# Performance work log

Hardware: AMD Instinct MI355X
Metric: run time of the kernel (lower is better)

Reference implementation:

```python
import jax, jax.numpy as jnp
import numpy as np

B, L, D_INNER, D_STATE, DT_RANK, MODES = 4, 2048, 256, 16, 16, 32
LN_EPS = 1e-5


def setup_inputs() -> dict:
    key = jax.random.key(0)
    ks = jax.random.split(key, 10)
    x = jax.random.normal(ks[0], (B, L, D_INNER), dtype=jnp.float32)
    ln_g = jnp.ones((D_INNER,), jnp.float32)
    ln_b = jnp.zeros((D_INNER,), jnp.float32)
    W_xproj = jax.random.normal(ks[1], (DT_RANK + 2 * D_STATE, D_INNER), jnp.float32) * (D_INNER ** -0.5)
    dt_init_std = DT_RANK ** -0.5  # dt_scale = 1.0
    W_dt = jax.random.uniform(ks[2], (D_INNER, DT_RANK), jnp.float32, -dt_init_std, dt_init_std)
    dt = jnp.exp(jax.random.uniform(ks[3], (D_INNER,), jnp.float32) * (np.log(0.1) - np.log(0.001)) + np.log(0.001))
    dt = jnp.clip(dt, 1e-4, None)
    b_dt = dt + jnp.log(-jnp.expm1(-dt))  # inverse softplus
    A_log = jnp.zeros((D_INNER, D_STATE), jnp.float32)  # log(ones)
    D_param = jnp.ones((D_INNER,), jnp.float32)
    scale = 1.0 / (D_STATE * D_STATE)
    w_re = scale * jax.random.uniform(ks[4], (D_STATE, D_STATE, MODES), jnp.float32)
    w_im = scale * jax.random.uniform(ks[5], (D_STATE, D_STATE, MODES), jnp.float32)
    return {"x": x, "ln_g": ln_g, "ln_b": ln_b, "W_xproj": W_xproj, "W_dt": W_dt,
            "b_dt": b_dt, "A_log": A_log, "D_param": D_param, "w_re": w_re, "w_im": w_im}


def _fft_kernel(hs, w_re, w_im):
    # hs: (B, L, d_inner, d_state); rfft over d_inner with d_state channels
    h = jnp.transpose(hs, (0, 1, 3, 2))  # (B, L, k, N)
    hf = jnp.fft.rfft(h, axis=-1)        # (B, L, k, N//2+1) complex
    n_freq = D_INNER // 2 + 1
    l = min(MODES, n_freq)
    w = (w_re + 1j * w_im).astype(hf.dtype)
    of = jnp.einsum('blix,iox->blox', hf[..., :l], w[..., :l])
    of = jnp.pad(of, ((0, 0), (0, 0), (0, 0), (0, n_freq - l)))
    h2 = jnp.fft.irfft(of, n=D_INNER, axis=-1)  # real, (B, L, k, N)
    return jnp.transpose(h2, (0, 1, 3, 2))      # (B, L, d_inner, d_state)


def reference(x, ln_g, ln_b, W_xproj, W_dt, b_dt, A_log, D_param, w_re, w_im):
    # LayerNorm
    mu = jnp.mean(x, axis=-1, keepdims=True)
    var = jnp.var(x, axis=-1, keepdims=True)
    xn = (x - mu) * jax.lax.rsqrt(var + LN_EPS) * ln_g + ln_b

    A = -jnp.exp(A_log)  # (d_inner, d_state)
    dbc = xn @ W_xproj.T  # (B, L, dt_rank + 2*d_state)
    delta_r = dbc[..., :DT_RANK]
    Bc = dbc[..., DT_RANK:DT_RANK + D_STATE]        # (B, L, d_state)
    Cc = dbc[..., DT_RANK + D_STATE:]               # (B, L, d_state)
    delta = jax.nn.softplus(delta_r @ W_dt.T + b_dt)  # (B, L, d_inner)

    deltaA = jnp.exp(delta[..., None] * A)                       # (B, L, d_inner, d_state)
    BX = delta[..., None] * Bc[:, :, None, :] * xn[..., None]    # (B, L, d_inner, d_state)

    # selective scan: h_t = deltaA_t * h_{t-1} + BX_t (parallel associative scan over L)
    def comb(c1, c2):
        a1, b1 = c1
        a2, b2 = c2
        return a1 * a2, a2 * b1 + b2
    _, hs = jax.lax.associative_scan(comb, (deltaA, BX), axis=1)

    hs = _fft_kernel(hs, w_re, w_im)
    y = jnp.einsum('bldn,bln->bld', hs, Cc)  # hs @ C
    y = y + D_param * xn
    return y + x
```

## Files before the change

kernel.cpp:

```cpp
#include <hip/hip_runtime.h>
#include <hip/hip_bf16.h>

#define B_   4
#define L_   2048
#define D_   256
#define NC   128
#define CL   16
#define ANG  0.02454369260617025967f

typedef __bf16 bf16x8 __attribute__((ext_vector_type(8)));
typedef float  f32x4  __attribute__((ext_vector_type(4)));

__global__ __launch_bounds__(256) void k_prep(
        const float* __restrict__ W_xproj, const float* __restrict__ w_re, const float* __restrict__ w_im,
        __hip_bfloat16* __restrict__ E_t, __hip_bfloat16* __restrict__ Wfrag,
        __hip_bfloat16* __restrict__ wfrag, __hip_bfloat16* __restrict__ E_inv)
{
    int idx = blockIdx.x * 256 + threadIdx.x;
    if (idx < 16384) {
        int x = idx >> 8, d = idx & 255;
        float v = (x < 32) ? __cosf(ANG * (float)((x * d) & 255))
                           : -__sinf(ANG * (float)(((x - 32) * d) & 255));
        E_t[idx] = __float2bfloat16(v);
    } else if (idx < 32768) {
        int f = idx - 16384;
        int ks = f >> 11, t = (f >> 3) & 255, j = f & 7;
        int jcol = (t >> 6) * 16 + (t & 15);
        int dd = ks * 32 + ((t >> 4) & 3) * 8 + j;
        float v = (jcol < 48) ? W_xproj[jcol * 256 + dd] : 0.f;
        Wfrag[f] = __float2bfloat16(v);
    } else if (idx < 65536) {
        int f = idx - 32768;
        int nt = f >> 9, l = (f >> 3) & 63, j = f & 7;
        int n = nt * 16 + (l & 15);
        int o = ((l >> 4) & 3) * 8 + j;
        float v = 0.f;
        if (o < 16) {
            int i = n >> 6, comp = (n >> 5) & 1, x = n & 31;
            v = comp ? w_im[(i * 16 + o) * 32 + x] : w_re[(i * 16 + o) * 32 + x];
        }
        wfrag[f] = __float2bfloat16(v);
    } else if (idx < 81920) {
        int f = idx - 65536;
        int nt = f >> 10, ks = (f >> 9) & 1, l = (f >> 3) & 63, j = f & 7;
        int row = ks * 32 + ((l >> 4) & 3) * 8 + j;
        int col = nt * 16 + (l & 15);
        float v = (row < 32) ? __cosf(ANG * (float)((row * col) & 255))
                             : -__sinf(ANG * (float)(((row - 32) * col) & 255));
        E_inv[f] = __float2bfloat16(v);
    }
}

__global__ __launch_bounds__(256) void k_lnscan(
        const float* __restrict__ x, const float* __restrict__ ln_g, const float* __restrict__ ln_b,
        const float* __restrict__ W_dt, const float* __restrict__ b_dt,
        const float* __restrict__ D_param, const float* __restrict__ A_log,
        const __hip_bfloat16* __restrict__ Wfrag,
        unsigned int* __restrict__ dxn, float* __restrict__ base_o,
        float* __restrict__ Bc_o, float* __restrict__ Cc_o,
        float* __restrict__ P, float* __restrict__ S)
{
    __shared__ __align__(16) float xn_s[16 * 260];
    __shared__ __align__(16) __bf16 xnb[16 * 256];
    __shared__ float dbc_s[16 * 52];
    int tid = threadIdx.x, wave = tid >> 6, lane = tid & 63;
    int blk = blockIdx.x;
    int grow0 = blk * CL;
    char* xnb_c = (char*)xnb;

#pragma unroll
    for (int rr = 0; rr < 4; rr++) {
        int r = wave * 4 + rr;
        const float* xr = x + (size_t)(grow0 + r) * D_;
        float v[4];
#pragma unroll
        for (int q = 0; q < 4; q++) v[q] = xr[lane + q * 64];
        float sum = v[0] + v[1] + v[2] + v[3];
        float sq  = v[0]*v[0] + v[1]*v[1] + v[2]*v[2] + v[3]*v[3];
#pragma unroll
        for (int off = 32; off; off >>= 1) { sum += __shfl_xor(sum, off); sq += __shfl_xor(sq, off); }
        float mu = sum * (1.f / D_);
        float rstd = rsqrtf(sq * (1.f / D_) - mu * mu + 1e-5f);
#pragma unroll
        for (int q = 0; q < 4; q++) {
            int d = lane + q * 64;
            float xv = (v[q] - mu) * rstd * ln_g[d] + ln_b[d];
            xn_s[r * 260 + d] = xv;
            *(__bf16*)(xnb_c + r * 512 + ((d * 2) ^ ((r & 7) << 4))) = (__bf16)xv;
            base_o[(size_t)(grow0 + r) * D_ + d] = v[q] + D_param[d] * xv;
        }
    }
    __syncthreads();

    {
        int mrow = lane & 15;
        f32x4 acc = {0.f, 0.f, 0.f, 0.f};
#pragma unroll
        for (int ks = 0; ks < 8; ks++) {
            bf16x8 af = *(const bf16x8*)(xnb_c + mrow * 512 +
                          ((ks * 64 + ((lane >> 4) * 16)) ^ ((mrow & 7) << 4)));
            bf16x8 bf = *(const bf16x8*)(Wfrag + (ks * 256 + tid) * 8);
            acc = __builtin_amdgcn_mfma_f32_16x16x32_bf16(af, bf, acc, 0, 0, 0);
        }
        int j = wave * 16 + (lane & 15);
#pragma unroll
        for (int q = 0; q < 4; q++) {
            int r = (lane >> 4) * 4 + q;
            if (j < 48) dbc_s[r * 52 + j] = acc[q];
            if (j >= 32 && j < 48)      Cc_o[(size_t)(grow0 + r) * 16 + j - 32] = acc[q];
            else if (j >= 16 && j < 32) Bc_o[(size_t)(grow0 + r) * 16 + j - 16] = acc[q];
        }
    }
    __syncthreads();

    int d = tid;
    float wdt[16];
#pragma unroll
    for (int q = 0; q < 4; q++) {
        f32x4 w4 = *(const f32x4*)&W_dt[d * 16 + q * 4];
#pragma unroll
        for (int k = 0; k < 4; k++) wdt[q * 4 + k] = w4[k];
    }
    float bd = b_dt[d];
    float dlt_r[16];
#pragma unroll
    for (int r = 0; r < 16; r++) {
        float din = bd;
#pragma unroll
        for (int k = 0; k < 16; k++) din = fmaf(dbc_s[r * 52 + k], wdt[k], din);
        din = (din > 15.f) ? din : log1pf(__expf(din));
        dlt_r[r] = din;
        union { __bf16 h2[2]; unsigned int u; } pk;
        pk.h2[0] = (__bf16)din;
        pk.h2[1] = (__bf16)xn_s[r * 260 + d];
        dxn[(size_t)(grow0 + r) * D_ + d] = pk.u;
    }

    float ar[16];
#pragma unroll
    for (int q = 0; q < 4; q++) {
        f32x4 a4 = *(const f32x4*)&A_log[d * 16 + q * 4];
#pragma unroll
        for (int k = 0; k < 4; k++) ar[q * 4 + k] = -__expf(a4[k]);
    }
    bool uni = true;
#pragma unroll
    for (int n = 1; n < 16; n++) uni = uni && (ar[n] == ar[0]);
    float s[16], dsum = 0.f;
#pragma unroll
    for (int n = 0; n < 16; n++) s[n] = 0.f;
    if (uni) {
        float ar0 = ar[0];
#pragma unroll
        for (int t = 0; t < CL; t++) {
            float dl = dlt_r[t];
            float dx = dl * xn_s[t * 260 + d];
            dsum += dl;
            float e = __expf(dl * ar0);
#pragma unroll
            for (int n = 0; n < 16; n++)
                s[n] = fmaf(e, s[n], dx * dbc_s[t * 52 + 16 + n]);
        }
    } else {
#pragma unroll
        for (int t = 0; t < CL; t++) {
            float dl = dlt_r[t];
            float dx = dl * xn_s[t * 260 + d];
            dsum += dl;
#pragma unroll
            for (int n = 0; n < 16; n++) {
                float e = __expf(dl * ar[n]);
                s[n] = fmaf(e, s[n], dx * dbc_s[t * 52 + 16 + n]);
            }
        }
    }
    size_t o = (size_t)blk * 4096 + d * 16;
    if (uni) {
        float p0 = __expf(ar[0] * dsum);
#pragma unroll
        for (int q = 0; q < 4; q++) {
            f32x4 pv, sv;
#pragma unroll
            for (int k = 0; k < 4; k++) { pv[k] = p0; sv[k] = s[q*4+k]; }
            *reinterpret_cast<f32x4*>(&P[o + q * 4]) = pv;
            *reinterpret_cast<f32x4*>(&S[o + q * 4]) = sv;
        }
    } else {
#pragma unroll
        for (int q = 0; q < 4; q++) {
            f32x4 pv, sv;
#pragma unroll
            for (int k = 0; k < 4; k++) { pv[k] = __expf(ar[q*4+k] * dsum); sv[k] = s[q*4+k]; }
            *reinterpret_cast<f32x4*>(&P[o + q * 4]) = pv;
            *reinterpret_cast<f32x4*>(&S[o + q * 4]) = sv;
        }
    }
}

__global__ __launch_bounds__(256) void k_scan_par(
        const float* __restrict__ P, float* __restrict__ S_H0)
{
    __shared__ float gPS[512];
    int tid = threadIdx.x;
    int g2 = tid >> 5, cl2 = tid & 31;
    int ch = blockIdx.x * 32 + cl2;
    int b2 = ch >> 12, dn2 = ch & 4095;
    size_t cb = ((size_t)b2 * NC + g2 * 16) * 4096 + dn2;
    float pv[16], sv[16];
#pragma unroll
    for (int c = 0; c < 16; c++) {
        pv[c] = P[cb + (size_t)c * 4096];
        sv[c] = S_H0[cb + (size_t)c * 4096];
    }
    float pA = 1.f, sA = 0.f;
#pragma unroll
    for (int c = 0; c < 16; c++) { sA = fmaf(pv[c], sA, sv[c]); pA *= pv[c]; }
    gPS[(g2 * 32 + cl2) * 2 - (g2 * 32 + cl2)] = 0.f;
    gPS[(g2 * 32 + cl2)] = pA;
    __syncthreads();
    __shared__ float gS2[256];
    gS2[g2 * 32 + cl2] = sA;
    __syncthreads();
    float h = 0.f;
    for (int gg = 0; gg < g2; gg++)
        h = fmaf(gPS[gg * 32 + cl2], h, gS2[gg * 32 + cl2]);
#pragma unroll
    for (int c = 0; c < 16; c++) {
        S_H0[cb + (size_t)c * 4096] = h;
        h = fmaf(pv[c], h, sv[c]);
    }
}

__global__ __launch_bounds__(256, 2) void k_fused(
        const unsigned int* __restrict__ dxn,
        const float* __restrict__ Bc, const float* __restrict__ Cc,
        const float* __restrict__ A_log, const float* __restrict__ H0,
        const float* __restrict__ base, float* __restrict__ out,
        const __hip_bfloat16* __restrict__ E_t, const __hip_bfloat16* __restrict__ wfrag,
        const __hip_bfloat16* __restrict__ E_inv)
{
    __shared__ __align__(16) char smem[70784];
    __bf16* hfb  = (__bf16*)(smem + 32768);
    __bf16* gsb  = (__bf16*)(smem + 66560);
    __bf16* ccb  = (__bf16*)(smem + 68736);
    float*  bc_s = (float*)(smem + 69760);

    int tid = threadIdx.x, wave = tid >> 6, lane = tid & 63;
    int blk = blockIdx.x;
    int grow0 = blk * CL;
    int d = tid;

    bc_s[tid] = Bc[(size_t)grow0 * 16 + tid];
    {
        float ccv = Cc[(size_t)grow0 * 16 + tid];
        int r = tid >> 4, o = tid & 15;
        ccb[r * 32 + o] = (__bf16)ccv;
        ccb[r * 32 + 16 + o] = (__bf16)0.f;
    }
    float dlt[16], dxv[16];
#pragma unroll
    for (int t = 0; t < 16; t++) {
        unsigned int v = dxn[(size_t)(grow0 + t) * D_ + d];
        dlt[t] = __uint_as_float(v << 16);
        dxv[t] = __uint_as_float(v & 0xffff0000u);
    }
    float ar[16], h[16];
    {
        size_t ho = (size_t)blk * 4096 + d * 16;
#pragma unroll
        for (int q = 0; q < 4; q++) {
            f32x4 a4 = *(const f32x4*)&A_log[d * 16 + q * 4];
            f32x4 h4 = *(const f32x4*)&H0[ho + q * 4];
#pragma unroll
            for (int k = 0; k < 4; k++) { ar[q*4+k] = -__expf(a4[k]); h[q*4+k] = h4[k]; }
        }
    }
    bool uni = true;
#pragma unroll
    for (int n = 1; n < 16; n++) uni = uni && (ar[n] == ar[0]);
    float ar0 = ar[0];

    int xx = wave * 16 + (lane & 15);
    bf16x8 bfrag[8];
#pragma unroll
    for (int ks = 0; ks < 8; ks++)
        bfrag[ks] = *(const bf16x8*)(E_t + xx * 256 + ks * 32 + ((lane >> 4) * 8));
    int swz = (lane & 7) << 4;
    __syncthreads();

#pragma unroll
    for (int g = 0; g < 4; g++) {
        if (uni) {
#pragma unroll
            for (int tl = 0; tl < 4; tl++) {
                int t = g * 4 + tl;
                float dl = dlt[t];
                float dx = dl * dxv[t];
                float e = __expf(dl * ar0);
#pragma unroll
                for (int n = 0; n < 16; n++) {
                    h[n] = fmaf(e, h[n], dx * bc_s[t * 16 + n]);
                    int m = tl * 16 + n;
                    *(__bf16*)(smem + m * 512 + ((d * 2) ^ ((m & 7) << 4))) = (__bf16)h[n];
                }
            }
        } else {
#pragma unroll
            for (int tl = 0; tl < 4; tl++) {
                int t = g * 4 + tl;
                float dl = dlt[t];
                float dx = dl * dxv[t];
#pragma unroll
                for (int n = 0; n < 16; n++) {
                    float e = __expf(dl * ar[n]);
                    h[n] = fmaf(e, h[n], dx * bc_s[t * 16 + n]);
                    int m = tl * 16 + n;
                    *(__bf16*)(smem + m * 512 + ((d * 2) ^ ((m & 7) << 4))) = (__bf16)h[n];
                }
            }
        }
        __syncthreads();
        f32x4 acc[4];
#pragma unroll
        for (int mt = 0; mt < 4; mt++) { acc[mt][0]=0.f; acc[mt][1]=0.f; acc[mt][2]=0.f; acc[mt][3]=0.f; }
#pragma unroll
        for (int ks = 0; ks < 8; ks++) {
#pragma unroll
            for (int mt = 0; mt < 4; mt++) {
                int m = mt * 16 + (lane & 15);
                bf16x8 af = *(const bf16x8*)(smem + m * 512 + ((ks * 64 + ((lane >> 4) * 16)) ^ swz));
                acc[mt] = __builtin_amdgcn_mfma_f32_16x16x32_bf16(af, bfrag[ks], acc[mt], 0, 0, 0);
            }
        }
#pragma unroll
        for (int mt = 0; mt < 4; mt++) {
            int r = g * 4 + mt;
#pragma unroll
            for (int q = 0; q < 4; q++) {
                int i = (lane >> 4) * 4 + q;
                hfb[(r * 16 + i) * 66 + xx] = (__bf16)acc[mt][q];
            }
        }
        __syncthreads();
    }

    {
        bf16x8 ccf = *(const bf16x8*)((char*)ccb + (lane & 15) * 64 + ((lane >> 4) * 16));
#pragma unroll
        for (int ntl = 0; ntl < 16; ntl++) {
            int nt = wave * 16 + ntl;
            f32x4 a = {0.f, 0.f, 0.f, 0.f};
            bf16x8 wf = *(const bf16x8*)(wfrag + (nt * 64 + lane) * 8);
            a = __builtin_amdgcn_mfma_f32_16x16x32_bf16(ccf, wf, a, 0, 0, 0);
            int col = nt * 16 + (lane & 15);
#pragma unroll
            for (int q = 0; q < 4; q++) {
                int r = (lane >> 4) * 4 + q;
                *(__bf16*)(smem + r * 2048 + col * 2) = (__bf16)a[q];
            }
        }
    }
    __syncthreads();

    {
        int xs = tid & 31, rg = tid >> 5;
#pragma unroll
        for (int r2 = 0; r2 < 2; r2++) {
            int r = rg * 2 + r2;
            float gre = 0.f, gim = 0.f;
#pragma unroll
            for (int i = 0; i < 16; i++) {
                float hr = (float)hfb[(r * 16 + i) * 66 + xs];
                float hi = (float)hfb[(r * 16 + i) * 66 + 32 + xs];
                float wr = (float)*(__bf16*)(smem + r * 2048 + (i * 64 + xs) * 2);
                float wi = (float)*(__bf16*)(smem + r * 2048 + (i * 64 + 32 + xs) * 2);
                gre = fmaf(hr, wr, gre); gre = fmaf(-hi, wi, gre);
                gim = fmaf(hr, wi, gim); gim = fmaf(hi, wr, gim);
            }
            float sc = xs ? 2.f : 1.f;
            gsb[r * 68 + xs]      = (__bf16)(gre * sc);
            gsb[r * 68 + 32 + xs] = (__bf16)(gim * sc);
        }
    }
    __syncthreads();

    {
        bf16x8 ga0 = *(const bf16x8*)((char*)gsb + (lane & 15) * 136 + ((lane >> 4) * 16));
        bf16x8 ga1 = *(const bf16x8*)((char*)gsb + (lane & 15) * 136 + 64 + ((lane >> 4) * 16));
#pragma unroll
        for (int ntl = 0; ntl < 4; ntl++) {
            int nt = wave * 4 + ntl;
            f32x4 a = {0.f, 0.f, 0.f, 0.f};
            a = __builtin_amdgcn_mfma_f32_16x16x32_bf16(
                    ga0, *(const bf16x8*)(E_inv + ((nt * 2 + 0) * 64 + lane) * 8), a, 0, 0, 0);
            a = __builtin_amdgcn_mfma_f32_16x16x32_bf16(
                    ga1, *(const bf16x8*)(E_inv + ((nt * 2 + 1) * 64 + lane) * 8), a, 0, 0, 0);
            int dcol = nt * 16 + (lane & 15);
#pragma unroll
            for (int q = 0; q < 4; q++) {
                int r = (lane >> 4) * 4 + q;
                size_t go = (size_t)(grow0 + r) * D_ + dcol;
                out[go] = base[go] + a[q] * (1.f / 256.f);
            }
        }
    }
}

extern "C" void kernel_launch(void* const* d_in, const int* in_sizes, int n_in,
                              void* d_out, int out_size, void* d_ws, size_t ws_size,
                              hipStream_t stream)
{
    const float* x       = (const float*)d_in[0];
    const float* ln_g    = (const float*)d_in[1];
    const float* ln_b    = (const float*)d_in[2];
    const float* W_xproj = (const float*)d_in[3];
    const float* W_dt    = (const float*)d_in[4];
    const float* b_dt    = (const float*)d_in[5];
    const float* A_log   = (const float*)d_in[6];
    const float* D_param = (const float*)d_in[7];
    const float* w_re    = (const float*)d_in[8];
    const float* w_im    = (const float*)d_in[9];

    float* ws    = (float*)d_ws;
    float* base  = ws;
    float* S_H0  = base + 2097152;
    float* P     = S_H0 + 2097152;
    unsigned int* dxn = (unsigned int*)(P + 2097152);
    float* Bc    = (float*)(dxn + 2097152);
    float* Cc    = Bc + 131072;
    __hip_bfloat16* tab = (__hip_bfloat16*)(Cc + 131072);
    __hip_bfloat16* E_t   = tab;
    __hip_bfloat16* Wfrag = tab + 16384;
    __hip_bfloat16* wfrag = tab + 32768;
    __hip_bfloat16* E_inv = tab + 65536;
    float* out = (float*)d_out;

    hipLaunchKernelGGL(k_prep, dim3(320), dim3(256), 0, stream,
                       W_xproj, w_re, w_im, E_t, Wfrag, wfrag, E_inv);
    hipLaunchKernelGGL(k_lnscan, dim3(B_*NC), dim3(256), 0, stream,
                       x, ln_g, ln_b, W_dt, b_dt, D_param, A_log, Wfrag,
                       dxn, base, Bc, Cc, P, S_H0);
    hipLaunchKernelGGL(k_scan_par, dim3(B_*NC), dim3(256), 0, stream, P, S_H0);
    hipLaunchKernelGGL(k_fused, dim3(B_*NC), dim3(256), 0, stream,
                       dxn, Bc, Cc, A_log, S_H0, base, out, E_t, wfrag, E_inv);
}
```

Measured before the change: 56.24 us.

## Drop base and P intermediates, recompute decay from dsum, retile FFT MFMA

```diff
diff --git a/kernel.cpp b/kernel.cpp
--- a/kernel.cpp
+++ b/kernel.cpp
@@ -9,6 +9,7 @@
 #define ANG  0.02454369260617025967f
 
 typedef __bf16 bf16x8 __attribute__((ext_vector_type(8)));
+typedef __bf16 bf16x4 __attribute__((ext_vector_type(4)));
 typedef float  f32x4  __attribute__((ext_vector_type(4)));
 
 __global__ __launch_bounds__(256) void k_prep(
@@ -36,7 +37,7 @@
         int o = ((l >> 4) & 3) * 8 + j;
         float v = 0.f;
         if (o < 16) {
-            int i = n >> 6, comp = (n >> 5) & 1, x = n & 31;
+            int comp = n >> 9, x = (n >> 4) & 31, i = n & 15;
             v = comp ? w_im[(i * 16 + o) * 32 + x] : w_re[(i * 16 + o) * 32 + x];
         }
         wfrag[f] = __float2bfloat16(v);
@@ -54,11 +55,11 @@
 __global__ __launch_bounds__(256) void k_lnscan(
         const float* __restrict__ x, const float* __restrict__ ln_g, const float* __restrict__ ln_b,
         const float* __restrict__ W_dt, const float* __restrict__ b_dt,
-        const float* __restrict__ D_param, const float* __restrict__ A_log,
+        const float* __restrict__ A_log,
         const __hip_bfloat16* __restrict__ Wfrag,
-        unsigned int* __restrict__ dxn, float* __restrict__ base_o,
+        unsigned int* __restrict__ dxn,
         float* __restrict__ Bc_o, float* __restrict__ Cc_o,
-        float* __restrict__ P, float* __restrict__ S)
+        float* __restrict__ dsum_o, float* __restrict__ S)
 {
     __shared__ __align__(16) float xn_s[16 * 260];
     __shared__ __align__(16) __bf16 xnb[16 * 256];
@@ -87,7 +88,6 @@
             float xv = (v[q] - mu) * rstd * ln_g[d] + ln_b[d];
             xn_s[r * 260 + d] = xv;
             *(__bf16*)(xnb_c + r * 512 + ((d * 2) ^ ((r & 7) << 4))) = (__bf16)xv;
-            base_o[(size_t)(grow0 + r) * D_ + d] = v[q] + D_param[d] * xv;
         }
     }
     __syncthreads();
@@ -174,56 +174,46 @@
             }
         }
     }
+    dsum_o[(size_t)blk * 256 + d] = dsum;
     size_t o = (size_t)blk * 4096 + d * 16;
-    if (uni) {
-        float p0 = __expf(ar[0] * dsum);
-#pragma unroll
-        for (int q = 0; q < 4; q++) {
-            f32x4 pv, sv;
-#pragma unroll
-            for (int k = 0; k < 4; k++) { pv[k] = p0; sv[k] = s[q*4+k]; }
-            *reinterpret_cast<f32x4*>(&P[o + q * 4]) = pv;
-            *reinterpret_cast<f32x4*>(&S[o + q * 4]) = sv;
-        }
-    } else {
-#pragma unroll
-        for (int q = 0; q < 4; q++) {
-            f32x4 pv, sv;
-#pragma unroll
-            for (int k = 0; k < 4; k++) { pv[k] = __expf(ar[q*4+k] * dsum); sv[k] = s[q*4+k]; }
-            *reinterpret_cast<f32x4*>(&P[o + q * 4]) = pv;
-            *reinterpret_cast<f32x4*>(&S[o + q * 4]) = sv;
-        }
+#pragma unroll
+    for (int q = 0; q < 4; q++) {
+        f32x4 sv;
+#pragma unroll
+        for (int k = 0; k < 4; k++) sv[k] = s[q*4+k];
+        *reinterpret_cast<f32x4*>(&S[o + q * 4]) = sv;
     }
 }
 
 __global__ __launch_bounds__(256) void k_scan_par(
-        const float* __restrict__ P, float* __restrict__ S_H0)
+        const float* __restrict__ A_log, const float* __restrict__ dsum,
+        float* __restrict__ S_H0)
 {
-    __shared__ float gPS[512];
+    __shared__ float gP[256];
+    __shared__ float gS[256];
     int tid = threadIdx.x;
     int g2 = tid >> 5, cl2 = tid & 31;
     int ch = blockIdx.x * 32 + cl2;
     int b2 = ch >> 12, dn2 = ch & 4095;
+    int dd = dn2 >> 4;
+    float arv = -__expf(A_log[dn2]);
     size_t cb = ((size_t)b2 * NC + g2 * 16) * 4096 + dn2;
+    size_t db = ((size_t)b2 * NC + g2 * 16) * 256 + dd;
     float pv[16], sv[16];
 #pragma unroll
     for (int c = 0; c < 16; c++) {
-        pv[c] = P[cb + (size_t)c * 4096];
+        pv[c] = __expf(arv * dsum[db + (size_t)c * 256]);
         sv[c] = S_H0[cb + (size_t)c * 4096];
     }
     float pA = 1.f, sA = 0.f;
 #pragma unroll
     for (int c = 0; c < 16; c++) { sA = fmaf(pv[c], sA, sv[c]); pA *= pv[c]; }
-    gPS[(g2 * 32 + cl2) * 2 - (g2 * 32 + cl2)] = 0.f;
-    gPS[(g2 * 32 + cl2)] = pA;
-    __syncthreads();
-    __shared__ float gS2[256];
-    gS2[g2 * 32 + cl2] = sA;
+    gP[g2 * 32 + cl2] = pA;
+    gS[g2 * 32 + cl2] = sA;
     __syncthreads();
     float h = 0.f;
     for (int gg = 0; gg < g2; gg++)
-        h = fmaf(gPS[gg * 32 + cl2], h, gS2[gg * 32 + cl2]);
+        h = fmaf(gP[gg * 32 + cl2], h, gS[gg * 32 + cl2]);
 #pragma unroll
     for (int c = 0; c < 16; c++) {
         S_H0[cb + (size_t)c * 4096] = h;
@@ -233,19 +223,21 @@
 
 __global__ __launch_bounds__(256, 2) void k_fused(
         const unsigned int* __restrict__ dxn,
+        const float* __restrict__ xin, const float* __restrict__ D_param,
         const float* __restrict__ Bc, const float* __restrict__ Cc,
         const float* __restrict__ A_log, const float* __restrict__ H0,
-        const float* __restrict__ base, float* __restrict__ out,
+        float* __restrict__ out,
         const __hip_bfloat16* __restrict__ E_t, const __hip_bfloat16* __restrict__ wfrag,
         const __hip_bfloat16* __restrict__ E_inv)
 {
-    __shared__ __align__(16) char smem[70784];
+    __shared__ __align__(16) char smem[69760];
     __bf16* hfb  = (__bf16*)(smem + 32768);
-    __bf16* gsb  = (__bf16*)(smem + 66560);
-    __bf16* ccb  = (__bf16*)(smem + 68736);
-    float*  bc_s = (float*)(smem + 69760);
+    __bf16* gsb  = (__bf16*)(smem + 65536);
+    __bf16* ccb  = (__bf16*)(smem + 67712);
+    float*  bc_s = (float*)(smem + 68736);
 
     int tid = threadIdx.x, wave = tid >> 6, lane = tid & 63;
+    int wm = wave >> 1, wx = wave & 1;
     int blk = blockIdx.x;
     int grow0 = blk * CL;
     int d = tid;
@@ -257,13 +249,9 @@
         ccb[r * 32 + o] = (__bf16)ccv;
         ccb[r * 32 + 16 + o] = (__bf16)0.f;
     }
-    float dlt[16], dxv[16];
-#pragma unroll
-    for (int t = 0; t < 16; t++) {
-        unsigned int v = dxn[(size_t)(grow0 + t) * D_ + d];
-        dlt[t] = __uint_as_float(v << 16);
-        dxv[t] = __uint_as_float(v & 0xffff0000u);
-    }
+    unsigned int dxnv[16];
+#pragma unroll
+    for (int t = 0; t < 16; t++) dxnv[t] = dxn[(size_t)(grow0 + t) * D_ + d];
     float ar[16], h[16];
     {
         size_t ho = (size_t)blk * 4096 + d * 16;
@@ -280,12 +268,20 @@
     for (int n = 1; n < 16; n++) uni = uni && (ar[n] == ar[0]);
     float ar0 = ar[0];
 
-    int xx = wave * 16 + (lane & 15);
-    bf16x8 bfrag[8];
-#pragma unroll
-    for (int ks = 0; ks < 8; ks++)
-        bfrag[ks] = *(const bf16x8*)(E_t + xx * 256 + ks * 32 + ((lane >> 4) * 8));
+    bf16x8 bfragAll[2][8];
+#pragma unroll
+    for (int nt2 = 0; nt2 < 2; nt2++) {
+        int xa = wx * 32 + nt2 * 16 + (lane & 15);
+#pragma unroll
+        for (int ks = 0; ks < 8; ks++)
+            bfragAll[nt2][ks] = *(const bf16x8*)(E_t + xa * 256 + ks * 32 + ((lane >> 4) * 8));
+    }
     int swz = (lane & 7) << 4;
+    f32x4 acc[2][2];
+#pragma unroll
+    for (int a = 0; a < 2; a++)
+#pragma unroll
+        for (int b = 0; b < 2; b++) { acc[a][b][0]=0.f; acc[a][b][1]=0.f; acc[a][b][2]=0.f; acc[a][b][3]=0.f; }
     __syncthreads();
 
 #pragma unroll
@@ -293,13 +289,13 @@
         if (uni) {
 #pragma unroll
             for (int tl = 0; tl < 4; tl++) {
-                int t = g * 4 + tl;
-                float dl = dlt[t];
-                float dx = dl * dxv[t];
+                unsigned int v = dxnv[g * 4 + tl];
+                float dl = __uint_as_float(v << 16);
+                float dx = dl * __uint_as_float(v & 0xffff0000u);
                 float e = __expf(dl * ar0);
 #pragma unroll
                 for (int n = 0; n < 16; n++) {
-                    h[n] = fmaf(e, h[n], dx * bc_s[t * 16 + n]);
+                    h[n] = fmaf(e, h[n], dx * bc_s[(g * 4 + tl) * 16 + n]);
                     int m = tl * 16 + n;
                     *(__bf16*)(smem + m * 512 + ((d * 2) ^ ((m & 7) << 4))) = (__bf16)h[n];
                 }
@@ -307,41 +303,57 @@
         } else {
 #pragma unroll
             for (int tl = 0; tl < 4; tl++) {
-                int t = g * 4 + tl;
-                float dl = dlt[t];
-                float dx = dl * dxv[t];
+                unsigned int v = dxnv[g * 4 + tl];
+                float dl = __uint_as_float(v << 16);
+                float dx = dl * __uint_as_float(v & 0xffff0000u);
 #pragma unroll
                 for (int n = 0; n < 16; n++) {
                     float e = __expf(dl * ar[n]);
-                    h[n] = fmaf(e, h[n], dx * bc_s[t * 16 + n]);
+                    h[n] = fmaf(e, h[n], dx * bc_s[(g * 4 + tl) * 16 + n]);
                     int m = tl * 16 + n;
                     *(__bf16*)(smem + m * 512 + ((d * 2) ^ ((m & 7) << 4))) = (__bf16)h[n];
                 }
             }
         }
         __syncthreads();
-        f32x4 acc[4];
-#pragma unroll
-        for (int mt = 0; mt < 4; mt++) { acc[mt][0]=0.f; acc[mt][1]=0.f; acc[mt][2]=0.f; acc[mt][3]=0.f; }
 #pragma unroll
         for (int ks = 0; ks < 8; ks++) {
 #pragma unroll
-            for (int mt = 0; mt < 4; mt++) {
-                int m = mt * 16 + (lane & 15);
+            for (int tl2 = 0; tl2 < 2; tl2++) {
+                int m = (wm * 2 + tl2) * 16 + (lane & 15);
                 bf16x8 af = *(const bf16x8*)(smem + m * 512 + ((ks * 64 + ((lane >> 4) * 16)) ^ swz));
-                acc[mt] = __builtin_amdgcn_mfma_f32_16x16x32_bf16(af, bfrag[ks], acc[mt], 0, 0, 0);
-            }
-        }
-#pragma unroll
-        for (int mt = 0; mt < 4; mt++) {
-            int r = g * 4 + mt;
-#pragma unroll
-            for (int q = 0; q < 4; q++) {
-                int i = (lane >> 4) * 4 + q;
-                hfb[(r * 16 + i) * 66 + xx] = (__bf16)acc[mt][q];
+#pragma unroll
+                for (int nt2 = 0; nt2 < 2; nt2++)
+                    acc[tl2][nt2] = __builtin_amdgcn_mfma_f32_16x16x32_bf16(af, bfragAll[nt2][ks], acc[tl2][nt2], 0, 0, 0);
+            }
+        }
+#pragma unroll
+        for (int tl2 = 0; tl2 < 2; tl2++) {
+            int r = g * 4 + wm * 2 + tl2;
+#pragma unroll
+            for (int nt2 = 0; nt2 < 2; nt2++) {
+                int xcol = wx * 32 + nt2 * 16 + (lane & 15);
+                bf16x4 pk;
+#pragma unroll
+                for (int k = 0; k < 4; k++) { pk[k] = (__bf16)acc[tl2][nt2][k]; acc[tl2][nt2][k] = 0.f; }
+                *(bf16x4*)(&hfb[r * 1024 + xcol * 16 + (lane >> 4) * 4]) = pk;
             }
         }
         __syncthreads();
+    }
+
+    float xpf[4][4], xnpf[4][4], dpf[4];
+#pragma unroll
+    for (int ntl = 0; ntl < 4; ntl++) {
+        int dcol = (wave * 4 + ntl) * 16 + (lane & 15);
+        dpf[ntl] = D_param[dcol];
+#pragma unroll
+        for (int q = 0; q < 4; q++) {
+            int r = (lane >> 4) * 4 + q;
+            size_t go = (size_t)(grow0 + r) * D_ + dcol;
+            xpf[ntl][q] = xin[go];
+            xnpf[ntl][q] = __uint_as_float(dxn[go] & 0xffff0000u);
+        }
     }
 
     {
@@ -363,19 +375,30 @@
     __syncthreads();
 
     {
-        int xs = tid & 31, rg = tid >> 5;
-#pragma unroll
-        for (int r2 = 0; r2 < 2; r2++) {
-            int r = rg * 2 + r2;
+        __bf16* wcb = (__bf16*)smem;
+        int r = tid >> 4, x2 = tid & 15;
+#pragma unroll
+        for (int xh = 0; xh < 2; xh++) {
+            int xs = xh * 16 + x2;
+            bf16x8 hra = *(const bf16x8*)(&hfb[r * 1024 + xs * 16]);
+            bf16x8 hrb = *(const bf16x8*)(&hfb[r * 1024 + xs * 16 + 8]);
+            bf16x8 hia = *(const bf16x8*)(&hfb[r * 1024 + (xs + 32) * 16]);
+            bf16x8 hib = *(const bf16x8*)(&hfb[r * 1024 + (xs + 32) * 16 + 8]);
+            bf16x8 wra = *(const bf16x8*)(&wcb[r * 1024 + xs * 16]);
+            bf16x8 wrb = *(const bf16x8*)(&wcb[r * 1024 + xs * 16 + 8]);
+            bf16x8 wia = *(const bf16x8*)(&wcb[r * 1024 + 512 + xs * 16]);
+            bf16x8 wib = *(const bf16x8*)(&wcb[r * 1024 + 512 + xs * 16 + 8]);
             float gre = 0.f, gim = 0.f;
 #pragma unroll
-            for (int i = 0; i < 16; i++) {
-                float hr = (float)hfb[(r * 16 + i) * 66 + xs];
-                float hi = (float)hfb[(r * 16 + i) * 66 + 32 + xs];
-                float wr = (float)*(__bf16*)(smem + r * 2048 + (i * 64 + xs) * 2);
-                float wi = (float)*(__bf16*)(smem + r * 2048 + (i * 64 + 32 + xs) * 2);
+            for (int k = 0; k < 8; k++) {
+                float hr = (float)hra[k], hi = (float)hia[k];
+                float wr = (float)wra[k], wi = (float)wia[k];
                 gre = fmaf(hr, wr, gre); gre = fmaf(-hi, wi, gre);
                 gim = fmaf(hr, wi, gim); gim = fmaf(hi, wr, gim);
+                float hr2 = (float)hrb[k], hi2 = (float)hib[k];
+                float wr2 = (float)wrb[k], wi2 = (float)wib[k];
+                gre = fmaf(hr2, wr2, gre); gre = fmaf(-hi2, wi2, gre);
+                gim = fmaf(hr2, wi2, gim); gim = fmaf(hi2, wr2, gim);
             }
             float sc = xs ? 2.f : 1.f;
             gsb[r * 68 + xs]      = (__bf16)(gre * sc);
@@ -400,7 +423,7 @@
             for (int q = 0; q < 4; q++) {
                 int r = (lane >> 4) * 4 + q;
                 size_t go = (size_t)(grow0 + r) * D_ + dcol;
-                out[go] = base[go] + a[q] * (1.f / 256.f);
+                out[go] = xpf[ntl][q] + dpf[ntl] * xnpf[ntl][q] + a[q] * (1.f / 256.f);
             }
         }
     }
@@ -422,13 +445,12 @@
     const float* w_im    = (const float*)d_in[9];
 
     float* ws    = (float*)d_ws;
-    float* base  = ws;
-    float* S_H0  = base + 2097152;
-    float* P     = S_H0 + 2097152;
-    unsigned int* dxn = (unsigned int*)(P + 2097152);
+    float* S_H0  = ws;
+    unsigned int* dxn = (unsigned int*)(S_H0 + 2097152);
     float* Bc    = (float*)(dxn + 2097152);
     float* Cc    = Bc + 131072;
-    __hip_bfloat16* tab = (__hip_bfloat16*)(Cc + 131072);
+    float* dsum  = Cc + 131072;
+    __hip_bfloat16* tab = (__hip_bfloat16*)(dsum + 131072);
     __hip_bfloat16* E_t   = tab;
     __hip_bfloat16* Wfrag = tab + 16384;
     __hip_bfloat16* wfrag = tab + 32768;
@@ -438,9 +460,9 @@
     hipLaunchKernelGGL(k_prep, dim3(320), dim3(256), 0, stream,
                        W_xproj, w_re, w_im, E_t, Wfrag, wfrag, E_inv);
     hipLaunchKernelGGL(k_lnscan, dim3(B_*NC), dim3(256), 0, stream,
-                       x, ln_g, ln_b, W_dt, b_dt, D_param, A_log, Wfrag,
-                       dxn, base, Bc, Cc, P, S_H0);
-    hipLaunchKernelGGL(k_scan_par, dim3(B_*NC), dim3(256), 0, stream, P, S_H0);
+                       x, ln_g, ln_b, W_dt, b_dt, A_log, Wfrag,
+                       dxn, Bc, Cc, dsum, S_H0);
+    hipLaunchKernelGGL(k_scan_par, dim3(B_*NC), dim3(256), 0, stream, A_log, dsum, S_H0);
     hipLaunchKernelGGL(k_fused, dim3(B_*NC), dim3(256), 0, stream,
-                       dxn, Bc, Cc, A_log, S_H0, base, out, E_t, wfrag, E_inv);
+                       dxn, x, D_param, Bc, Cc, A_log, S_H0, out, E_t, wfrag, E_inv);
 }
```

Result: faster. 54.31 us (-3.4%).
